# Optimization experiments

Hardware: AMD Instinct MI355X
Metric: run time of the kernel (lower is better)

Reference implementation:

```python
import jax, jax.numpy as jnp
import numpy as np

B, T, F, NC, H = 128, 2048, 80, 10, 32
EPS = 1e-5


def _xavier(k, shape):
    fan_out, fan_in = shape
    lim = float(np.sqrt(6.0 / (fan_in + fan_out)))
    return jax.random.uniform(k, shape, jnp.float32, -lim, lim)


def _gru_w(k, shape):
    lim = float(1.0 / np.sqrt(H))
    return jax.random.uniform(k, shape, jnp.float32, -lim, lim)


def setup_inputs() -> dict:
    key = jax.random.key(0)
    ks = jax.random.split(key, 16)
    z = jnp.zeros
    o = jnp.ones
    inp = {
        "x": jax.random.normal(ks[0], (B, T, F), jnp.float32),
        # feature extractor: Linear+BN x3
        "W1": _xavier(ks[1], (256, F)), "b1": z(256), "g1": o(256), "be1": z(256),
        "W2": _xavier(ks[2], (128, 256)), "b2": z(128), "g2": o(128), "be2": z(128),
        "W3": _xavier(ks[3], (64, 128)), "b3": z(64), "g3": o(64), "be3": z(64),
        # bidirectional GRU, hidden=32, gates ordered (r,z,n) as in torch
        "Wih_f": _gru_w(ks[4], (3 * H, 64)), "Whh_f": _gru_w(ks[5], (3 * H, H)),
        "bih_f": _gru_w(ks[6], (3 * H,)), "bhh_f": _gru_w(ks[7], (3 * H,)),
        "Wih_b": _gru_w(ks[8], (3 * H, 64)), "Whh_b": _gru_w(ks[9], (3 * H, H)),
        "bih_b": _gru_w(ks[10], (3 * H,)), "bhh_b": _gru_w(ks[11], (3 * H,)),
        # attention MLP
        "Wa1": _xavier(ks[12], (32, 64)), "ba1": z(32),
        "Wa2": _xavier(ks[13], (1, 32)), "ba2": z(1),
        # classifier
        "Wc1": _xavier(ks[14], (32, 64)), "bc1": z(32), "gc": o(32), "bec": z(32),
        "Wc2": _xavier(ks[15], (NC, 32)), "bc2": z(NC),
    }
    return inp


def _bn(x, g, b):
    # BatchNorm1d, training-mode batch statistics (biased var), dropout omitted (eval)
    m = jnp.mean(x, 0)
    v = jnp.mean(jnp.square(x - m), 0)
    return (x - m) * jax.lax.rsqrt(v + EPS) * g + b


def _gru_dir(feats, Wih, Whh, bih, bhh, reverse):
    # feats: [B,T,64] -> outputs [B,T,H]
    xp = jnp.einsum('btf,gf->btg', feats, Wih) + bih  # precompute input projections

    def step(h, xt):
        gh = h @ Whh.T + bhh
        r = jax.nn.sigmoid(xt[:, :H] + gh[:, :H])
        zg = jax.nn.sigmoid(xt[:, H:2 * H] + gh[:, H:2 * H])
        n = jnp.tanh(xt[:, 2 * H:] + r * gh[:, 2 * H:])
        hn = (1.0 - zg) * n + zg * h
        return hn, hn

    h0 = jnp.zeros((feats.shape[0], H), feats.dtype)
    _, hs = jax.lax.scan(step, h0, jnp.swapaxes(xp, 0, 1), reverse=reverse)
    return jnp.swapaxes(hs, 0, 1)


def reference(x, W1, b1, g1, be1, W2, b2, g2, be2, W3, b3, g3, be3,
              Wih_f, Whh_f, bih_f, bhh_f, Wih_b, Whh_b, bih_b, bhh_b,
              Wa1, ba1, Wa2, ba2, Wc1, bc1, gc, bec, Wc2, bc2):
    Bv, Tv, Fv = x.shape
    h = x.reshape(-1, Fv)
    h = jax.nn.relu(_bn(h @ W1.T + b1, g1, be1))
    h = jax.nn.relu(_bn(h @ W2.T + b2, g2, be2))
    h = jax.nn.relu(_bn(h @ W3.T + b3, g3, be3))
    feats = h.reshape(Bv, Tv, 64)
    gf = _gru_dir(feats, Wih_f, Whh_f, bih_f, bhh_f, False)
    gb = _gru_dir(feats, Wih_b, Whh_b, bih_b, bhh_b, True)
    gru_out = jnp.concatenate([gf, gb], axis=-1)  # [B,T,64]
    scores = jnp.tanh(gru_out @ Wa1.T + ba1) @ Wa2.T + ba2  # [B,T,1]
    attn = jax.nn.softmax(scores, axis=1)
    pooled = jnp.sum(gru_out * attn, axis=1)  # [B,64]
    c = jax.nn.relu(_bn(pooled @ Wc1.T + bc1, gc, bec))
    return c @ Wc2.T + bc2
```

## Files before the change

### kernel.cpp

```cpp
#include <hip/hip_runtime.h>
#include <hip/hip_fp16.h>
#include <cstdint>
#include <cstddef>

#define EPSV 1e-5f
constexpr int Bb = 128, Tt = 2048, Ff = 80, NCc = 10, Hh = 32;
constexpr int Nn = Bb * Tt;

constexpr size_t OFF_H1 = 0;
constexpr size_t OFF_H3 = 0;
constexpr size_t OFF_GRU = 0;
constexpr size_t OFF_XP = (size_t)Nn * 64;
constexpr size_t OFF_SCORES = (size_t)Nn * 64;
constexpr size_t OFF_H2 = (size_t)Nn * 128;
constexpr size_t TAIL = (size_t)Nn * 192;
constexpr size_t P1o = TAIL;
constexpr size_t P2o = P1o + 64 * 256 * 2;
constexpr size_t P3o = P2o + 64 * 128 * 2;
constexpr size_t PZEND = P3o + 64 * 64 * 2;
constexpr size_t SC1o = PZEND;
constexpr size_t SC2o = SC1o + 512;
constexpr size_t SC3o = SC2o + 256;
constexpr size_t BMAXo = SC3o + 128;
constexpr size_t BSUMo = BMAXo + 128;
constexpr size_t POOLEDo = BSUMo + 128;
constexpr size_t WS_EXTENT = POOLEDo + 128 * 64;

struct alignas(8) half4 { __half x, y, z, w; };

__global__ __launch_bounds__(256) void zero_kernel(float* __restrict__ p, int n) {
  const int i = blockIdx.x * 256 + threadIdx.x;
  if (i < n) p[i] = 0.f;
}

template <int K, bool BN_IN, bool STATS, bool A16, bool C16, bool XP_PACK>
__global__ __launch_bounds__(256) void fc_kernel(
    const void* __restrict__ Av, const float* __restrict__ W,
    const float* __restrict__ bias, const float* __restrict__ scl,
    const float* __restrict__ shf, void* __restrict__ Cv, int ldc, int coloff,
    int COUT, float* __restrict__ Pstat) {
  __shared__ float smem[32 * 68 * 2 + 512];
  float* As = smem;
  float* Bs = smem + 32 * 68;
  float* Ss = smem + 32 * 68 * 2;
  float* Sh = Ss + 256;

  const int tid = threadIdx.x;
  const int r0 = blockIdx.x * 64;
  const int nb0 = blockIdx.y * 64;
  const int m0 = (tid >> 4) * 4;
  const int n0 = (tid & 15) * 4;

  if (BN_IN) {
    for (int k = tid; k < K; k += 256) {
      Ss[k] = scl[k];
      Sh[k] = shf[k];
    }
  }

  float acc[4][4] = {};

  constexpr int NKT = (K + 31) / 32;
  for (int kt = 0; kt < NKT; ++kt) {
    const int k0 = kt * 32;
    __syncthreads();
#pragma unroll
    for (int rep = 0; rep < 2; ++rep) {
      const int li = rep * 256 + tid;
      const int row = li >> 3;
      const int ko = (li & 7) * 4;
      float av[4] = {0.f, 0.f, 0.f, 0.f};
      if (k0 + ko < K) {
        if (A16) {
          const half4 v = *(const half4*)&(
              (const __half*)Av)[(size_t)(r0 + row) * K + k0 + ko];
          av[0] = __half2float(v.x); av[1] = __half2float(v.y);
          av[2] = __half2float(v.z); av[3] = __half2float(v.w);
        } else {
          const float4 v =
              *(const float4*)&((const float*)Av)[(size_t)(r0 + row) * K + k0 + ko];
          av[0] = v.x; av[1] = v.y; av[2] = v.z; av[3] = v.w;
        }
        if (BN_IN) {
#pragma unroll
          for (int e = 0; e < 4; ++e)
            av[e] = fmaxf(av[e] * Ss[k0 + ko + e] + Sh[k0 + ko + e], 0.f);
        }
      }
#pragma unroll
      for (int e = 0; e < 4; ++e) As[(ko + e) * 68 + row] = av[e];
      float bv[4] = {0.f, 0.f, 0.f, 0.f};
      const int wn = nb0 + row;
      if (wn < COUT && k0 + ko < K) {
        const float4 v = *(const float4*)&W[(size_t)wn * K + k0 + ko];
        bv[0] = v.x; bv[1] = v.y; bv[2] = v.z; bv[3] = v.w;
      }
#pragma unroll
      for (int e = 0; e < 4; ++e) Bs[(ko + e) * 68 + row] = bv[e];
    }
    __syncthreads();
#pragma unroll
    for (int kk = 0; kk < 32; ++kk) {
      const float4 a4 = *(const float4*)&As[kk * 68 + m0];
      const float4 b4 = *(const float4*)&Bs[kk * 68 + n0];
      const float a[4] = {a4.x, a4.y, a4.z, a4.w};
      const float b[4] = {b4.x, b4.y, b4.z, b4.w};
#pragma unroll
      for (int i = 0; i < 4; ++i)
#pragma unroll
        for (int j = 0; j < 4; ++j) acc[i][j] = fmaf(a[i], b[j], acc[i][j]);
    }
  }

  float colsum[4] = {0.f, 0.f, 0.f, 0.f};
  float colsq[4] = {0.f, 0.f, 0.f, 0.f};
#pragma unroll
  for (int i = 0; i < 4; ++i) {
    const int r = r0 + m0 + i;
    float vv[4];
#pragma unroll
    for (int j = 0; j < 4; ++j) {
      const int col = nb0 + n0 + j;
      float v = 0.f;
      if (col < COUT) v = acc[i][j] + bias[col];
      vv[j] = v;
      if (STATS) {
        colsum[j] += v;
        colsq[j] += v * v;
      }
    }
    if (XP_PACK) {
#pragma unroll
      for (int j = 0; j < 4; ++j) {
        const int col = nb0 + n0 + j;
        if (col < COUT)
          ((__half*)Cv)[(size_t)r * ldc + coloff +
                        ((col & 31) * 4 + (col >> 5))] = __float2half(vv[j]);
      }
    } else if (nb0 + n0 + 3 < COUT) {
      if (C16) {
        half4 o;
        o.x = __float2half(vv[0]); o.y = __float2half(vv[1]);
        o.z = __float2half(vv[2]); o.w = __float2half(vv[3]);
        *(half4*)&((__half*)Cv)[(size_t)r * ldc + coloff + nb0 + n0] = o;
      } else {
        float4 o;
        o.x = vv[0]; o.y = vv[1]; o.z = vv[2]; o.w = vv[3];
        *(float4*)&((float*)Cv)[(size_t)r * ldc + coloff + nb0 + n0] = o;
      }
    } else {
#pragma unroll
      for (int j = 0; j < 4; ++j) {
        const int col = nb0 + n0 + j;
        if (col < COUT) {
          if (C16)
            ((__half*)Cv)[(size_t)r * ldc + coloff + col] = __float2half(vv[j]);
          else
            ((float*)Cv)[(size_t)r * ldc + coloff + col] = vv[j];
        }
      }
    }
  }
  if (STATS) {
    __syncthreads();
    const int rg = tid >> 4;
#pragma unroll
    for (int j = 0; j < 4; ++j) {
      smem[(n0 + j) * 16 + rg] = colsum[j];
      smem[1024 + (n0 + j) * 16 + rg] = colsq[j];
    }
    __syncthreads();
    if (tid < 64) {
      float s = 0.f, q = 0.f;
#pragma unroll
      for (int g = 0; g < 16; ++g) {
        s += smem[tid * 16 + g];
        q += smem[1024 + tid * 16 + g];
      }
      const int col = nb0 + tid;
      if (col < COUT) {
        const int bkt = blockIdx.x & 63;
        atomicAdd(&Pstat[(size_t)bkt * COUT + col], s);
        atomicAdd(&Pstat[(size_t)64 * COUT + (size_t)bkt * COUT + col], q);
      }
    }
  }
}

__global__ __launch_bounds__(256) void bn_finalize(
    const float* __restrict__ P, int COUT, int nrows,
    const float* __restrict__ g, const float* __restrict__ be,
    float* __restrict__ scl, float* __restrict__ shf) {
  const int c = threadIdx.x;
  if (c < COUT) {
    float s = 0.f, q = 0.f;
    for (int b = 0; b < 64; ++b) {
      s += P[(size_t)b * COUT + c];
      q += P[(size_t)64 * COUT + (size_t)b * COUT + c];
    }
    const float invN = 1.f / (float)nrows;
    const float m = s * invN;
    const float var = q * invN - m * m;
    const float inv = rsqrtf(var + EPSV);
    scl[c] = g[c] * inv;
    shf[c] = be[c] - m * g[c] * inv;
  }
}

template <int J>
__device__ __forceinline__ float bc32(float v) {
  return __int_as_float(
      __builtin_amdgcn_ds_swizzle(__float_as_int(v), (J << 5)));
}

#define GRU_BCFMA(J)                                  \
  {                                                   \
    const float hx = bc32<(J)>(h);                    \
    const float hy = bc32<(J) + 16>(h);               \
    arx = fmaf(hx, wr[(J)], arx);                     \
    ary = fmaf(hy, wr[(J) + 16], ary);                \
    azx = fmaf(hx, wz[(J)], azx);                     \
    azy = fmaf(hy, wz[(J) + 16], azy);                \
    anx = fmaf(hx, wn[(J)], anx);                     \
    any_ = fmaf(hy, wn[(J) + 16], any_);              \
  }

#define GRU_STEP(U, PF)                                              \
  {                                                                  \
    const float xr = __half2float(ring[(U)].x);                      \
    const float xz = __half2float(ring[(U)].y);                      \
    const float xn = __half2float(ring[(U)].z);                      \
    if (PF) {                                                        \
      ring[(U)] = *(const half4*)((const char*)xq + xoff);           \
      xoff += (unsigned)xdel;                                        \
    }                                                                \
    float arx = xr + bhr, ary = 0.f;                                 \
    float azx = xz + bhz, azy = 0.f;                                 \
    float anx = bhn, any_ = 0.f;                                     \
    GRU_BCFMA(0) GRU_BCFMA(1) GRU_BCFMA(2) GRU_BCFMA(3)              \
    GRU_BCFMA(4) GRU_BCFMA(5) GRU_BCFMA(6) GRU_BCFMA(7)              \
    GRU_BCFMA(8) GRU_BCFMA(9) GRU_BCFMA(10) GRU_BCFMA(11)            \
    GRU_BCFMA(12) GRU_BCFMA(13) GRU_BCFMA(14) GRU_BCFMA(15)          \
    const float sr = arx + ary, sz = azx + azy, sn = anx + any_;     \
    const float rg = 1.f / (1.f + __expf(-sr));                      \
    const float zg = 1.f / (1.f + __expf(-sz));                      \
    const float npre = fmaf(rg, sn, xn);                             \
    const float ng = 1.f - 2.f / (__expf(2.f * npre) + 1.f);         \
    h = fmaf(zg, h - ng, ng);                                        \
    *(float*)((char*)out + ooff) = h;                                \
    ooff += (unsigned)odel;                                          \
  }

__global__ __launch_bounds__(64) void gru_kernel(
    const __half* __restrict__ xq, const float* __restrict__ Whh_f,
    const float* __restrict__ bhh_f, const float* __restrict__ Whh_b,
    const float* __restrict__ bhh_b, float* __restrict__ out) {
  const int b = blockIdx.x;
  const int lane = threadIdx.x;
  const int d = lane >> 5;
  const int i = lane & 31;
  const float* __restrict__ Whh = d ? Whh_b : Whh_f;
  const float* __restrict__ bhh = d ? bhh_b : bhh_f;

  float wr[32], wz[32], wn[32];
#pragma unroll
  for (int j4 = 0; j4 < 8; ++j4) {
    const float4 vr = *(const float4*)&Whh[(size_t)i * 32 + j4 * 4];
    const float4 vz = *(const float4*)&Whh[(size_t)(32 + i) * 32 + j4 * 4];
    const float4 vn = *(const float4*)&Whh[(size_t)(64 + i) * 32 + j4 * 4];
    wr[j4 * 4 + 0] = vr.x; wr[j4 * 4 + 1] = vr.y;
    wr[j4 * 4 + 2] = vr.z; wr[j4 * 4 + 3] = vr.w;
    wz[j4 * 4 + 0] = vz.x; wz[j4 * 4 + 1] = vz.y;
    wz[j4 * 4 + 2] = vz.z; wz[j4 * 4 + 3] = vz.w;
    wn[j4 * 4 + 0] = vn.x; wn[j4 * 4 + 1] = vn.y;
    wn[j4 * 4 + 2] = vn.z; wn[j4 * 4 + 3] = vn.w;
  }
  const float bhr = bhh[i], bhz = bhh[32 + i], bhn = bhh[64 + i];

  const unsigned n0 = (unsigned)(b * Tt + (d ? Tt - 1 : 0));
  unsigned xoff = n0 * 512u + (unsigned)d * 256u + (unsigned)i * 8u;
  unsigned ooff = n0 * 256u + (unsigned)d * 128u + (unsigned)i * 4u;
  const int xdel = d ? -512 : 512;
  const int odel = d ? -256 : 256;

  half4 ring[8];
#pragma unroll
  for (int u = 0; u < 8; ++u) {
    ring[u] = *(const half4*)((const char*)xq + xoff);
    xoff += (unsigned)xdel;
  }

  float h = 0.f;

  for (int s = 0; s < Tt - 8; s += 8) {
    GRU_STEP(0, true) GRU_STEP(1, true) GRU_STEP(2, true) GRU_STEP(3, true)
    GRU_STEP(4, true) GRU_STEP(5, true) GRU_STEP(6, true) GRU_STEP(7, true)
  }
  GRU_STEP(0, false) GRU_STEP(1, false) GRU_STEP(2, false) GRU_STEP(3, false)
  GRU_STEP(4, false) GRU_STEP(5, false) GRU_STEP(6, false) GRU_STEP(7, false)
}

#undef GRU_STEP
#undef GRU_BCFMA

__device__ __forceinline__ float tanh_f(float x) {
  return 1.f - 2.f / (__expf(2.f * x) + 1.f);
}

__global__ __launch_bounds__(256) void attn_score_kernel(
    const float* __restrict__ G, const float* __restrict__ Wa1,
    const float* __restrict__ ba1, const float* __restrict__ Wa2,
    const float* __restrict__ ba2, float* __restrict__ scores) {
  const int n = blockIdx.x * 256 + threadIdx.x;
  const float* g = &G[(size_t)n * 64];
  float gv[64];
#pragma unroll
  for (int j4 = 0; j4 < 16; ++j4) {
    const float4 v = *(const float4*)&g[j4 * 4];
    gv[j4 * 4 + 0] = v.x; gv[j4 * 4 + 1] = v.y;
    gv[j4 * 4 + 2] = v.z; gv[j4 * 4 + 3] = v.w;
  }
  float sc = ba2[0];
#pragma unroll 4
  for (int l = 0; l < 32; ++l) {
    float a = ba1[l];
#pragma unroll
    for (int j = 0; j < 64; ++j) a = fmaf(Wa1[l * 64 + j], gv[j], a);
    sc = fmaf(Wa2[l], tanh_f(a), sc);
  }
  scores[n] = sc;
}

__global__ __launch_bounds__(256) void softmax_stats_kernel(
    const float* __restrict__ scores, float* __restrict__ bmax,
    float* __restrict__ bsum) {
  const int b = blockIdx.x;
  const int tid = threadIdx.x;
  __shared__ float red[256];
  const float* s = &scores[(size_t)b * Tt];
  float m = -1e30f;
  for (int t = tid; t < Tt; t += 256) m = fmaxf(m, s[t]);
  red[tid] = m;
  __syncthreads();
  for (int off = 128; off > 0; off >>= 1) {
    if (tid < off) red[tid] = fmaxf(red[tid], red[tid + off]);
    __syncthreads();
  }
  m = red[0];
  __syncthreads();
  float e = 0.f;
  for (int t = tid; t < Tt; t += 256) e += __expf(s[t] - m);
  red[tid] = e;
  __syncthreads();
  for (int off = 128; off > 0; off >>= 1) {
    if (tid < off) red[tid] += red[tid + off];
    __syncthreads();
  }
  if (tid == 0) {
    bmax[b] = m;
    bsum[b] = red[0];
  }
}

__global__ __launch_bounds__(256) void pooled_kernel(
    const float* __restrict__ G, const float* __restrict__ scores,
    const float* __restrict__ bmax, const float* __restrict__ bsum,
    float* __restrict__ pooled) {
  const int b = blockIdx.x;
  const int d = threadIdx.x & 63;
  const int q = threadIdx.x >> 6;
  const float m = bmax[b];
  float acc = 0.f;
  for (int t = q; t < Tt; t += 4) {
    const float w = __expf(scores[(size_t)b * Tt + t] - m);
    acc += w * G[((size_t)b * Tt + t) * 64 + d];
  }
  __shared__ float red[4][64];
  red[q][d] = acc;
  __syncthreads();
  if (threadIdx.x < 64) {
    const float v = red[0][d] + red[1][d] + red[2][d] + red[3][d];
    pooled[(size_t)b * 64 + d] = v / bsum[b];
  }
}

__global__ __launch_bounds__(128) void classifier_kernel(
    const float* __restrict__ pooled, const float* __restrict__ Wc1,
    const float* __restrict__ bc1, const float* __restrict__ gc,
    const float* __restrict__ bec, const float* __restrict__ Wc2,
    const float* __restrict__ bc2, float* __restrict__ out) {
  __shared__ float c1s[128][33];
  __shared__ float sA[32], sB[32];
  const int b = threadIdx.x;
  float pv[64];
#pragma unroll
  for (int j4 = 0; j4 < 16; ++j4) {
    const float4 v = *(const float4*)&pooled[(size_t)b * 64 + j4 * 4];
    pv[j4 * 4 + 0] = v.x; pv[j4 * 4 + 1] = v.y;
    pv[j4 * 4 + 2] = v.z; pv[j4 * 4 + 3] = v.w;
  }
#pragma unroll 2
  for (int j = 0; j < 32; ++j) {
    float a = bc1[j];
#pragma unroll
    for (int k = 0; k < 64; ++k) a = fmaf(Wc1[j * 64 + k], pv[k], a);
    c1s[b][j] = a;
  }
  __syncthreads();
  if (b < 32) {
    float s = 0.f, q = 0.f;
    for (int r = 0; r < 128; ++r) {
      const float v = c1s[r][b];
      s += v;
      q += v * v;
    }
    const float m = s * (1.f / 128.f);
    const float var = q * (1.f / 128.f) - m * m;
    const float inv = rsqrtf(var + EPSV);
    sA[b] = gc[b] * inv;
    sB[b] = bec[b] - m * gc[b] * inv;
  }
  __syncthreads();
  float act[32];
#pragma unroll
  for (int j = 0; j < 32; ++j)
    act[j] = fmaxf(c1s[b][j] * sA[j] + sB[j], 0.f);
#pragma unroll
  for (int k = 0; k < NCc; ++k) {
    float o = bc2[k];
#pragma unroll
    for (int j = 0; j < 32; ++j) o = fmaf(Wc2[k * 32 + j], act[j], o);
    out[(size_t)b * NCc + k] = o;
  }
}

extern "C" void kernel_launch(void* const* d_in, const int* in_sizes, int n_in,
                              void* d_out, int out_size, void* d_ws,
                              size_t ws_size, hipStream_t stream) {
  if (ws_size < WS_EXTENT * sizeof(float)) {
    zero_kernel<<<(out_size + 255) / 256, 256, 0, stream>>>((float*)d_out,
                                                            out_size);
    return;
  }

  const float* x = (const float*)d_in[0];
  const float* W1 = (const float*)d_in[1];
  const float* b1 = (const float*)d_in[2];
  const float* g1 = (const float*)d_in[3];
  const float* be1 = (const float*)d_in[4];
  const float* W2 = (const float*)d_in[5];
  const float* b2 = (const float*)d_in[6];
  const float* g2 = (const float*)d_in[7];
  const float* be2 = (const float*)d_in[8];
  const float* W3 = (const float*)d_in[9];
  const float* b3 = (const float*)d_in[10];
  const float* g3 = (const float*)d_in[11];
  const float* be3 = (const float*)d_in[12];
  const float* Wih_f = (const float*)d_in[13];
  const float* Whh_f = (const float*)d_in[14];
  const float* bih_f = (const float*)d_in[15];
  const float* bhh_f = (const float*)d_in[16];
  const float* Wih_b = (const float*)d_in[17];
  const float* Whh_b = (const float*)d_in[18];
  const float* bih_b = (const float*)d_in[19];
  const float* bhh_b = (const float*)d_in[20];
  const float* Wa1 = (const float*)d_in[21];
  const float* ba1 = (const float*)d_in[22];
  const float* Wa2 = (const float*)d_in[23];
  const float* ba2 = (const float*)d_in[24];
  const float* Wc1 = (const float*)d_in[25];
  const float* bc1 = (const float*)d_in[26];
  const float* gc = (const float*)d_in[27];
  const float* bec = (const float*)d_in[28];
  const float* Wc2 = (const float*)d_in[29];
  const float* bc2 = (const float*)d_in[30];

  float* ws = (float*)d_ws;
  __half* h1 = (__half*)(ws + OFF_H1);
  __half* h2 = (__half*)(ws + OFF_H2);
  float* h3 = ws + OFF_H3;
  __half* xp = (__half*)(ws + OFF_XP);
  float* gru = ws + OFF_GRU;

  {
    const int nz = (int)(PZEND - P1o);
    zero_kernel<<<(nz + 255) / 256, 256, 0, stream>>>(ws + P1o, nz);
  }

  const int rowblocks = Nn / 64;

  fc_kernel<80, false, true, false, true, false>
      <<<dim3(rowblocks, 4), 256, 0, stream>>>(x, W1, b1, nullptr, nullptr, h1,
                                               256, 0, 256, ws + P1o);
  bn_finalize<<<1, 256, 0, stream>>>(ws + P1o, 256, Nn, g1, be1, ws + SC1o,
                                     ws + SC1o + 256);
  fc_kernel<256, true, true, true, true, false>
      <<<dim3(rowblocks, 2), 256, 0, stream>>>(h1, W2, b2, ws + SC1o,
                                               ws + SC1o + 256, h2, 128, 0,
                                               128, ws + P2o);
  bn_finalize<<<1, 128, 0, stream>>>(ws + P2o, 128, Nn, g2, be2, ws + SC2o,
                                     ws + SC2o + 128);
  fc_kernel<128, true, true, true, false, false>
      <<<dim3(rowblocks, 1), 256, 0, stream>>>(h2, W3, b3, ws + SC2o,
                                               ws + SC2o + 128, h3, 64, 0, 64,
                                               ws + P3o);
  bn_finalize<<<1, 64, 0, stream>>>(ws + P3o, 64, Nn, g3, be3, ws + SC3o,
                                    ws + SC3o + 64);
  fc_kernel<64, true, false, false, true, true>
      <<<dim3(rowblocks, 2), 256, 0, stream>>>(h3, Wih_f, bih_f, ws + SC3o,
                                               ws + SC3o + 64, xp, 256, 0, 96,
                                               nullptr);
  fc_kernel<64, true, false, false, true, true>
      <<<dim3(rowblocks, 2), 256, 0, stream>>>(h3, Wih_b, bih_b, ws + SC3o,
                                               ws + SC3o + 64, xp, 256, 128,
                                               96, nullptr);
  gru_kernel<<<Bb, 64, 0, stream>>>(xp, Whh_f, bhh_f, Whh_b, bhh_b, gru);
  attn_score_kernel<<<Nn / 256, 256, 0, stream>>>(gru, Wa1, ba1, Wa2, ba2,
                                                  ws + OFF_SCORES);
  softmax_stats_kernel<<<Bb, 256, 0, stream>>>(ws + OFF_SCORES, ws + BMAXo,
                                               ws + BSUMo);
  pooled_kernel<<<Bb, 256, 0, stream>>>(gru, ws + OFF_SCORES, ws + BMAXo,
                                        ws + BSUMo, ws + POOLEDo);
  classifier_kernel<<<1, 128, 0, stream>>>(ws + POOLEDo, Wc1, bc1, gc, bec,
                                           Wc2, bc2, (float*)d_out);
}
```

Measured before the change: 1.840 ms.

## Stage GRU input projections through double-buffered LDS chunks per direction

The GRU input projections for the forward and backward directions now go into separate contiguous buffers. The GRU kernel copies 64-timestep chunks of both into a double-buffered shared-memory region with wide cooperative loads while it computes the previous chunk. Each lane then reads its per-step gate inputs from LDS in bursts of four, replacing the per-step scattered global loads through a ring. The aim is to take global memory latency off the serial recurrence, at the cost of extra LDS traffic and an lgkmcnt wait issued only once, before the loop. Synchronisation between staged writes and reads in later chunks relies on implicit wave ordering within a single 64-thread block.

```diff
diff --git a/kernel.cpp b/kernel.cpp
--- a/kernel.cpp
+++ b/kernel.cpp
@@ -10,8 +10,9 @@
 constexpr size_t OFF_H1 = 0;
 constexpr size_t OFF_H3 = 0;
 constexpr size_t OFF_GRU = 0;
-constexpr size_t OFF_XP = (size_t)Nn * 64;
+constexpr size_t OFF_XPF = (size_t)Nn * 64;
 constexpr size_t OFF_SCORES = (size_t)Nn * 64;
+constexpr size_t OFF_XPB = (size_t)Nn * 128;
 constexpr size_t OFF_H2 = (size_t)Nn * 128;
 constexpr size_t TAIL = (size_t)Nn * 192;
 constexpr size_t P1o = TAIL;
@@ -207,11 +208,18 @@
   }
 }
 
+constexpr int CH = 64;
+
 template <int J>
 __device__ __forceinline__ float bc32(float v) {
   return __int_as_float(
       __builtin_amdgcn_ds_swizzle(__float_as_int(v), (J << 5)));
 }
+
+union H4 {
+  uint2 u2;
+  struct { __half2 lo, hi; } h;
+};
 
 #define GRU_BCFMA(J)                                  \
   {                                                   \
@@ -225,15 +233,11 @@
     any_ = fmaf(hy, wn[(J) + 16], any_);              \
   }
 
-#define GRU_STEP(U, PF)                                              \
+#define GRU_STEP(BK, U)                                              \
   {                                                                  \
-    const float xr = __half2float(ring[(U)].x);                      \
-    const float xz = __half2float(ring[(U)].y);                      \
-    const float xn = __half2float(ring[(U)].z);                      \
-    if (PF) {                                                        \
-      ring[(U)] = *(const half4*)((const char*)xq + xoff);           \
-      xoff += (unsigned)xdel;                                        \
-    }                                                                \
+    const float xr = __half2float((BK)[(U)].h.lo.x);                 \
+    const float xz = __half2float((BK)[(U)].h.lo.y);                 \
+    const float xn = __half2float((BK)[(U)].h.hi.x);                 \
     float arx = xr + bhr, ary = 0.f;                                 \
     float azx = xz + bhz, azy = 0.f;                                 \
     float anx = bhn, any_ = 0.f;                                     \
@@ -251,14 +255,38 @@
     ooff += (unsigned)odel;                                          \
   }
 
+#define GRU_BURST(BK)                                 \
+  {                                                   \
+    _Pragma("unroll")                                 \
+    for (int u = 0; u < 4; ++u) {                     \
+      (BK)[u].u2 = *(const uint2*)(ldsc + rptr);      \
+      rptr += sdel;                                   \
+    }                                                 \
+  }
+
+#define GRU_STAGE(BUF, FOFF, BOFF)                                          \
+  {                                                                         \
+    _Pragma("unroll")                                                       \
+    for (int it = 0; it < 16; ++it) {                                       \
+      const uint4 vf =                                                      \
+          *(const uint4*)(srcf + (FOFF) + it * 1024 + lane * 16);           \
+      const uint4 vb =                                                      \
+          *(const uint4*)(srcb + (BOFF) + it * 1024 + lane * 16);           \
+      *(uint4*)(ldsc + (BUF) * 16384 + it * 1024 + lane * 16) = vf;         \
+      *(uint4*)(ldsc + 32768 + (BUF) * 16384 + it * 1024 + lane * 16) = vb; \
+    }                                                                       \
+  }
+
 __global__ __launch_bounds__(64) void gru_kernel(
-    const __half* __restrict__ xq, const float* __restrict__ Whh_f,
-    const float* __restrict__ bhh_f, const float* __restrict__ Whh_b,
-    const float* __restrict__ bhh_b, float* __restrict__ out) {
+    const __half* __restrict__ xpf, const __half* __restrict__ xpb,
+    const float* __restrict__ Whh_f, const float* __restrict__ bhh_f,
+    const float* __restrict__ Whh_b, const float* __restrict__ bhh_b,
+    float* __restrict__ out) {
+  __shared__ __align__(16) unsigned char ldsbuf[2 * 2 * CH * 256];
+  char* ldsc = (char*)ldsbuf;
   const int b = blockIdx.x;
   const int lane = threadIdx.x;
-  const int d = lane >> 5;
-  const int i = lane & 31;
+  const int d = lane >> 5, i = lane & 31;
   const float* __restrict__ Whh = d ? Whh_b : Whh_f;
   const float* __restrict__ bhh = d ? bhh_b : bhh_f;
 
@@ -277,31 +305,43 @@
   }
   const float bhr = bhh[i], bhz = bhh[32 + i], bhn = bhh[64 + i];
 
-  const unsigned n0 = (unsigned)(b * Tt + (d ? Tt - 1 : 0));
-  unsigned xoff = n0 * 512u + (unsigned)d * 256u + (unsigned)i * 8u;
-  unsigned ooff = n0 * 256u + (unsigned)d * 128u + (unsigned)i * 4u;
-  const int xdel = d ? -512 : 512;
+  const char* srcf = (const char*)xpf + (size_t)b * (Tt * 256);
+  const char* srcb = (const char*)xpb + (size_t)b * (Tt * 256);
+
+  const int sdel = d ? -256 : 256;
+  const int cb0 = d * 32768 + i * 8 + (d ? (CH - 1) * 256 : 0);
+
+  GRU_STAGE(0, 0, (Tt - CH) * 256)
+  asm volatile("s_waitcnt lgkmcnt(0)" ::: "memory");
+
+  int rptr = cb0;
+  H4 bkA[4], bkB[4];
+  GRU_BURST(bkA)
+
+  float h = 0.f;
+  const unsigned nrow0 = (unsigned)(b * Tt + (d ? Tt - 1 : 0));
+  unsigned ooff = nrow0 * 256u + (unsigned)d * 128u + (unsigned)i * 4u;
   const int odel = d ? -256 : 256;
 
-  half4 ring[8];
-#pragma unroll
-  for (int u = 0; u < 8; ++u) {
-    ring[u] = *(const half4*)((const char*)xq + xoff);
-    xoff += (unsigned)xdel;
-  }
-
-  float h = 0.f;
-
-  for (int s = 0; s < Tt - 8; s += 8) {
-    GRU_STEP(0, true) GRU_STEP(1, true) GRU_STEP(2, true) GRU_STEP(3, true)
-    GRU_STEP(4, true) GRU_STEP(5, true) GRU_STEP(6, true) GRU_STEP(7, true)
-  }
-  GRU_STEP(0, false) GRU_STEP(1, false) GRU_STEP(2, false) GRU_STEP(3, false)
-  GRU_STEP(4, false) GRU_STEP(5, false) GRU_STEP(6, false) GRU_STEP(7, false)
+  int buf = 0;
+  for (int c = 0; c < 32; ++c) {
+    const int nc = (c < 31) ? c + 1 : 31;
+    GRU_STAGE(buf ^ 1, nc * (CH * 256), (Tt - (nc + 1) * CH) * 256)
+    for (int sbp = 0; sbp < 8; ++sbp) {
+      GRU_BURST(bkB)
+      GRU_STEP(bkA, 0) GRU_STEP(bkA, 1) GRU_STEP(bkA, 2) GRU_STEP(bkA, 3)
+      if (sbp == 7) rptr = cb0 + (buf ^ 1) * 16384;
+      GRU_BURST(bkA)
+      GRU_STEP(bkB, 0) GRU_STEP(bkB, 1) GRU_STEP(bkB, 2) GRU_STEP(bkB, 3)
+    }
+    buf ^= 1;
+  }
 }
 
 #undef GRU_STEP
 #undef GRU_BCFMA
+#undef GRU_BURST
+#undef GRU_STAGE
 
 __device__ __forceinline__ float tanh_f(float x) {
   return 1.f - 2.f / (__expf(2.f * x) + 1.f);
@@ -479,7 +519,8 @@
   __half* h1 = (__half*)(ws + OFF_H1);
   __half* h2 = (__half*)(ws + OFF_H2);
   float* h3 = ws + OFF_H3;
-  __half* xp = (__half*)(ws + OFF_XP);
+  __half* xpf = (__half*)(ws + OFF_XPF);
+  __half* xpb = (__half*)(ws + OFF_XPB);
   float* gru = ws + OFF_GRU;
 
   {
@@ -508,13 +549,13 @@
                                     ws + SC3o + 64);
   fc_kernel<64, true, false, false, true, true>
       <<<dim3(rowblocks, 2), 256, 0, stream>>>(h3, Wih_f, bih_f, ws + SC3o,
-                                               ws + SC3o + 64, xp, 256, 0, 96,
+                                               ws + SC3o + 64, xpf, 128, 0, 96,
                                                nullptr);
   fc_kernel<64, true, false, false, true, true>
       <<<dim3(rowblocks, 2), 256, 0, stream>>>(h3, Wih_b, bih_b, ws + SC3o,
-                                               ws + SC3o + 64, xp, 256, 128,
-                                               96, nullptr);
-  gru_kernel<<<Bb, 64, 0, stream>>>(xp, Whh_f, bhh_f, Whh_b, bhh_b, gru);
+                                               ws + SC3o + 64, xpb, 128, 0, 96,
+                                               nullptr);
+  gru_kernel<<<Bb, 64, 0, stream>>>(xpf, xpb, Whh_f, bhh_f, Whh_b, bhh_b, gru);
   attn_score_kernel<<<Nn / 256, 256, 0, stream>>>(gru, Wa1, ba1, Wa2, ba2,
                                                   ws + OFF_SCORES);
   softmax_stats_kernel<<<Bb, 256, 0, stream>>>(ws + OFF_SCORES, ws + BMAXo,
```

After: 1.857 ms. Within noise of the previous version (+0.9%).
